# Optimization experiments

Measured on AMD Instinct MI355X. Metric: run time of the kernel, lower is better.

Reference implementation:

```python
import jax, jax.numpy as jnp
import numpy as np

B, NV, C = 4, 32768, 128
NCLS, K = 10, 500
GRID = 180  # spatial extent at feature_map_stride=8 (1440/8)
STRIDE = 8.0
PCR = np.array([-54.0, -54.0, -5.0, 54.0, 54.0, 3.0], np.float32)
VOX = np.array([0.075, 0.075, 0.2], np.float32)
LIMIT = np.array([-61.2, -61.2, -10.0, 61.2, 61.2, 10.0], np.float32)
SCORE_THRESH = 0.1
BN_EPS = 1e-5


def setup_inputs() -> dict:
    key = jax.random.key(0)
    ks = jax.random.split(key, 24)
    s = 1.0 / np.sqrt(C)
    inp = {}
    inp['feats'] = jax.random.normal(ks[0], (B * NV, C), jnp.float32)
    inp['voxel_xy'] = jax.random.randint(ks[1], (B * NV, 2), 0, GRID, dtype=jnp.int32)
    inp['W1'] = jax.random.normal(ks[2], (6, C, C), jnp.float32) * s
    inp['b1'] = jax.random.normal(ks[3], (6, C), jnp.float32) * 0.01
    inp['bn_gamma'] = 1.0 + 0.1 * jax.random.normal(ks[4], (6, C), jnp.float32)
    inp['bn_beta'] = 0.1 * jax.random.normal(ks[5], (6, C), jnp.float32)
    inp['bn_mean'] = 0.1 * jax.random.normal(ks[6], (6, C), jnp.float32)
    inp['bn_var'] = 0.5 + jax.random.uniform(ks[7], (6, C), jnp.float32)
    outs = [('hm', NCLS), ('center', 2), ('center_z', 1), ('dim', 3), ('rot', 2), ('vel', 2)]
    for i, (name, oc) in enumerate(outs):
        sc = 0.05 if name == 'dim' else s  # keep dim.exp() in a sane range
        inp['W2_' + name] = jax.random.normal(ks[8 + 2 * i], (C, oc), jnp.float32) * sc
        inp['b2_' + name] = jax.random.normal(ks[9 + 2 * i], (oc,), jnp.float32) * 0.01
    inp['batch_size'] = B
    return inp


def _forward(feats, voxel_xy, W1, b1, bn_gamma, bn_beta, bn_mean, bn_var,
             W2_hm, b2_hm, W2_center, b2_center, W2_center_z, b2_center_z,
             W2_dim, b2_dim, W2_rot, b2_rot, W2_vel, b2_vel, batch_size):
    Bs = batch_size
    N = feats.shape[0]
    Nv = N // Bs
    # --- separate heads: SubMConv2d(k=1)==per-voxel linear; BN in eval mode ---
    h = jnp.einsum('nc,bcd->bnd', feats, W1) + b1[:, None, :]            # [6,N,C]
    inv = bn_gamma / jnp.sqrt(bn_var + BN_EPS)
    h = jax.nn.relu((h - bn_mean[:, None, :]) * inv[:, None, :] + bn_beta[:, None, :])
    hm = jax.nn.sigmoid(h[0] @ W2_hm + b2_hm)                            # [N,NCLS]
    center = h[1] @ W2_center + b2_center                                # [N,2]
    center_z = h[2] @ W2_center_z + b2_center_z                          # [N,1]
    dim = jnp.exp(h[3] @ W2_dim + b2_dim)                                # [N,3]
    rot = h[4] @ W2_rot + b2_rot                                         # [N,2] (cos,sin)
    vel = h[5] @ W2_vel + b2_vel                                         # [N,2]
    # --- CenterNet-style decode (nuscenes _topk_1d): per-class topk then global topk ---
    hm_b = hm.reshape(Bs, Nv, NCLS)
    sc_c, idx_c = jax.lax.top_k(jnp.transpose(hm_b, (0, 2, 1)), K)       # [B,NCLS,K]
    topk_score, topk_ind = jax.lax.top_k(sc_c.reshape(Bs, NCLS * K), K)  # [B,K]
    class_ids = topk_ind // K                                            # [B,K]
    vox_ind = jnp.take_along_axis(idx_c.reshape(Bs, NCLS * K), topk_ind, axis=1)  # [B,K] in [0,Nv)

    def gather(x):  # x: [N,d] -> [B,K,d]
        return jnp.take_along_axis(x.reshape(Bs, Nv, -1), vox_ind[:, :, None], axis=1)

    ctr = gather(center)
    cz = gather(center_z)
    dm = gather(dim)
    rt = gather(rot)
    vl = gather(vel)
    xy = gather(voxel_xy.astype(jnp.float32))
    angle = jnp.arctan2(rt[..., 1:2], rt[..., 0:1])
    xs = (xy[..., 0:1] + ctr[..., 0:1]) * STRIDE * VOX[0] + PCR[0]
    ys = (xy[..., 1:2] + ctr[..., 1:2]) * STRIDE * VOX[1] + PCR[1]
    boxes = jnp.concatenate([xs, ys, cz, dm, angle, vl], axis=-1)        # [B,K,9]
    lim = jnp.asarray(LIMIT)
    mask = (jnp.all(boxes[..., :3] >= lim[:3], axis=-1)
            & jnp.all(boxes[..., :3] <= lim[3:], axis=-1)
            & (topk_score > SCORE_THRESH))                               # [B,K]
    boxes_scores = jnp.concatenate([boxes, topk_score[..., None]], -1) * mask[..., None].astype(boxes.dtype)
    labels = jnp.where(mask, class_ids + 1, 0)                           # class_id_mapping identity, +1
    voxel_ids = vox_ind + (jnp.arange(Bs, dtype=vox_ind.dtype) * Nv)[:, None]  # global add_features ids
    return boxes_scores, labels, voxel_ids, mask


def reference(feats, voxel_xy, W1, b1, bn_gamma, bn_beta, bn_mean, bn_var,
              W2_hm, b2_hm, W2_center, b2_center, W2_center_z, b2_center_z,
              W2_dim, b2_dim, W2_rot, b2_rot, W2_vel, b2_vel, batch_size):
    return _forward(feats, voxel_xy, W1, b1, bn_gamma, bn_beta, bn_mean, bn_var,
                    W2_hm, b2_hm, W2_center, b2_center, W2_center_z, b2_center_z,
                    W2_dim, b2_dim, W2_rot, b2_rot, W2_vel, b2_vel, batch_size)
```

## Files before the change

kernel.cpp:

```cpp
#include <hip/hip_runtime.h>
#include <math.h>

#define NV 32768
#define CD 128
#define NCLS 10
#define KSEL 500
#define BNEPS 1e-5f
#define NK (NCLS * NV)
#define H20CUT 0x3E000
#define H20BINS 6144
#define CANDCAP 2048
#define NCHUNK 64
#define CHUNKV (NK / NCHUNK)
#define CHUNK4 (CHUNKV / 4)

__global__ __launch_bounds__(256, 3) void stageA_kernel(
    const float* __restrict__ feats,
    const float* __restrict__ W1,
    const float* __restrict__ b1,
    const float* __restrict__ bng,
    const float* __restrict__ bnb,
    const float* __restrict__ bnm,
    const float* __restrict__ bnv,
    const float* __restrict__ W2hm,
    const float* __restrict__ b2hm,
    unsigned int* __restrict__ scoreb,
    unsigned int* __restrict__ zbase,
    int zwords)
{
    __shared__ __align__(16) float smem[64 * 129];
    __shared__ float w2s[CD * NCLS];
    __shared__ float b2s[NCLS];
    float4* const fsmv = (float4*)smem;

    const int tid = threadIdx.x;
    const int gbase = blockIdx.x * 64;

    if (blockIdx.x == 0) {
        for (int i = tid; i < zwords; i += 256) zbase[i] = 0u;
    }

    for (int i = tid; i < CD * NCLS; i += 256) w2s[i] = W2hm[i];
    if (tid < NCLS) b2s[tid] = b2hm[tid];

    for (int t = tid; t < 64 * 32; t += 256) {
        const int r = t >> 5;
        const int g = t & 31;
        const float4 v = *(const float4*)(feats + (((size_t)(gbase + r)) << 7) + (g << 2));
        fsmv[r * 32 + (g ^ (r & 31))] = v;
    }
    __syncthreads();

    const int c0 = (tid & 15) << 3;
    const int r0 = (tid >> 4) << 2;
    const float* const Wc0 = W1 + c0;

    float acc[4][8];
    #pragma unroll
    for (int i = 0; i < 4; ++i)
        #pragma unroll
        for (int j = 0; j < 8; ++j) acc[i][j] = 0.f;

    float4 frA[4], frB[4], wA[8], wB[8];

    #pragma unroll
    for (int i = 0; i < 4; ++i) {
        const int row = r0 + i;
        frA[i] = fsmv[row * 32 + (0 ^ (row & 31))];
    }
    #pragma unroll
    for (int kk = 0; kk < 4; ++kk) {
        wA[2 * kk]     = *(const float4*)(Wc0 + (kk << 7));
        wA[2 * kk + 1] = *(const float4*)(Wc0 + (kk << 7) + 4);
    }

#define SA_PREFETCH(FR, WW, KC)                                           \
    {                                                                     \
        const int kc_ = (KC);                                             \
        _Pragma("unroll")                                                 \
        for (int i = 0; i < 4; ++i) {                                     \
            const int row = r0 + i;                                       \
            FR[i] = fsmv[row * 32 + (kc_ ^ (row & 31))];                  \
        }                                                                 \
        const int kb_ = kc_ << 2;                                         \
        _Pragma("unroll")                                                 \
        for (int kk = 0; kk < 4; ++kk) {                                  \
            WW[2 * kk]     = *(const float4*)(Wc0 + ((kb_ + kk) << 7));   \
            WW[2 * kk + 1] = *(const float4*)(Wc0 + ((kb_ + kk) << 7) + 4); \
        }                                                                 \
    }

#define SA_COMPUTE(FR, WW)                                                \
    {                                                                     \
        const float* frp = (const float*)FR;                              \
        const float* wp  = (const float*)WW;                              \
        _Pragma("unroll")                                                 \
        for (int kk = 0; kk < 4; ++kk)                                    \
            _Pragma("unroll")                                             \
            for (int ri = 0; ri < 4; ++ri) {                              \
                const float f = frp[ri * 4 + kk];                         \
                _Pragma("unroll")                                         \
                for (int ci = 0; ci < 8; ++ci)                            \
                    acc[ri][ci] = fmaf(f, wp[kk * 8 + ci], acc[ri][ci]);  \
            }                                                             \
    }

    for (int kc = 0; kc < 32; kc += 2) {
        SA_PREFETCH(frB, wB, kc + 1)
        SA_COMPUTE(frA, wA)
        SA_PREFETCH(frA, wA, (kc + 2) & 31)
        SA_COMPUTE(frB, wB)
    }
#undef SA_PREFETCH
#undef SA_COMPUTE

    __syncthreads();

    #pragma unroll
    for (int ci = 0; ci < 8; ++ci) {
        const int c = c0 + ci;
        const float inv = bng[c] / sqrtf(bnv[c] + BNEPS);
        const float mu = bnm[c];
        const float be = bnb[c];
        const float bb = b1[c];
        #pragma unroll
        for (int ri = 0; ri < 4; ++ri) {
            const float h = (acc[ri][ci] + bb - mu) * inv + be;
            acc[ri][ci] = fmaxf(h, 0.f);
        }
    }
    #pragma unroll
    for (int ri = 0; ri < 4; ++ri)
        #pragma unroll
        for (int ci = 0; ci < 8; ++ci)
            smem[(r0 + ri) * 129 + c0 + ci] = acc[ri][ci];
    __syncthreads();

    const int r = tid & 63;
    const int ogrp = tid >> 6;
    float lg[3] = {0.f, 0.f, 0.f};
    for (int c = 0; c < 128; ++c) {
        const float a = smem[r * 129 + c];
        #pragma unroll
        for (int i = 0; i < 3; ++i) {
            const int o = ogrp + 4 * i;
            if (o < NCLS) lg[i] = fmaf(a, w2s[c * NCLS + o], lg[i]);
        }
    }
    const int n = gbase + r;
    const int b = n >> 15;
    const int v = n & (NV - 1);
    unsigned int* sb = scoreb + (size_t)b * NK;
    #pragma unroll
    for (int i = 0; i < 3; ++i) {
        const int o = ogrp + 4 * i;
        if (o < NCLS) {
            const float x = lg[i] + b2s[o];
            const float s = 1.f / (1.f + expf(-x));
            sb[o * NV + v] = __float_as_uint(s);
        }
    }
}

__global__ __launch_bounds__(256) void stageB1_kernel(
    const unsigned int* __restrict__ scoreb,
    unsigned int* __restrict__ hist20)
{
    __shared__ unsigned int lh[H20BINS];
    const int tid = threadIdx.x;
    const int b = blockIdx.y;
    const uint4* sb4 = (const uint4*)(scoreb + (size_t)b * NK) + (size_t)blockIdx.x * CHUNK4;

    for (int i = tid; i < H20BINS; i += 256) lh[i] = 0u;
    __syncthreads();

    #pragma unroll
    for (int q = 0; q < 5; ++q) {
        const uint4 v = sb4[q * 256 + tid];
        const unsigned int sv[4] = {v.x, v.y, v.z, v.w};
        #pragma unroll
        for (int k = 0; k < 4; ++k) {
            const int rel = (int)(sv[k] >> 12) - H20CUT;
            if (rel >= 0) atomicAdd(&lh[rel], 1u);
        }
    }
    __syncthreads();

    unsigned int* gh = hist20 + (size_t)b * H20BINS;
    for (int i = tid; i < H20BINS; i += 256) {
        const unsigned int v = lh[i];
        if (v) atomicAdd(&gh[i], v);
    }
}

__global__ __launch_bounds__(256) void stageB2_kernel(
    const unsigned int* __restrict__ scoreb,
    const unsigned int* __restrict__ hist20,
    unsigned int* __restrict__ cnt,
    unsigned long long* __restrict__ cand)
{
    __shared__ unsigned int hh[H20BINS];
    __shared__ unsigned int part[256];
    __shared__ unsigned int sT;
    const int tid = threadIdx.x;
    const int b = blockIdx.y;

    const unsigned int* gh = hist20 + (size_t)b * H20BINS;
    for (int i = tid; i < H20BINS; i += 256) hh[i] = gh[i];
    __syncthreads();

    unsigned int Ls = 0;
    #pragma unroll
    for (int i = 0; i < 24; ++i) Ls += hh[tid * 24 + i];
    part[tid] = Ls;
    __syncthreads();

    for (int off = 1; off < 256; off <<= 1) {
        const unsigned int add = (tid + off < 256) ? part[tid + off] : 0u;
        __syncthreads();
        part[tid] += add;
        __syncthreads();
    }
    const unsigned int incl = part[tid];
    const unsigned int above_seg = incl - Ls;

    if (above_seg < KSEL && incl >= KSEL) {
        int above = (int)above_seg;
        int tbin = tid * 24;
        for (int i = 23; i >= 0; --i) {
            const int c = (int)hh[tid * 24 + i];
            if (above + c >= KSEL) { tbin = tid * 24 + i; break; }
            above += c;
        }
        sT = ((unsigned int)(tbin + H20CUT)) << 12;
    }
    if (tid == 0 && incl < KSEL) sT = ((unsigned int)H20CUT) << 12;
    __syncthreads();
    const unsigned int T = sT;

    const uint4* sb4 = (const uint4*)(scoreb + (size_t)b * NK) + (size_t)blockIdx.x * CHUNK4;
    #pragma unroll
    for (int q = 0; q < 5; ++q) {
        const int vi = q * 256 + tid;
        const uint4 v = sb4[vi];
        const unsigned int sv[4] = {v.x, v.y, v.z, v.w};
        const unsigned int i0 = (unsigned int)((blockIdx.x * CHUNK4 + vi) * 4);
        #pragma unroll
        for (int k = 0; k < 4; ++k) {
            if (sv[k] >= T) {
                const unsigned int p = atomicAdd(&cnt[b], 1u);
                if (p < CANDCAP)
                    cand[(size_t)b * CANDCAP + p] =
                        ((unsigned long long)sv[k] << 32) |
                        (unsigned long long)(0xFFFFFFFFu - (i0 + k));
            }
        }
    }
}

__global__ __launch_bounds__(1024) void stageB3_kernel(
    const unsigned long long* __restrict__ cand,
    const unsigned int* __restrict__ cnt,
    float* __restrict__ sel_score,
    int* __restrict__ sel_cls,
    int* __restrict__ sel_vox)
{
    __shared__ unsigned long long kbuf[CANDCAP];
    const int b = blockIdx.x;
    const int tid = threadIdx.x;
    const int n = min((int)cnt[b], CANDCAP);
    int m = 512;
    while (m < n) m <<= 1;
    for (int i = tid; i < m; i += 1024)
        kbuf[i] = (i < n) ? cand[(size_t)b * CANDCAP + i] : 0ull;
    __syncthreads();
    for (int size = 2; size <= m; size <<= 1) {
        for (int stride = size >> 1; stride > 0; stride >>= 1) {
            for (int j = tid; j < m; j += 1024) {
                const int p = j ^ stride;
                if (p > j) {
                    const unsigned long long x = kbuf[j];
                    const unsigned long long y = kbuf[p];
                    const bool descRegion = ((j & size) == 0);
                    if ((x < y) == descRegion) { kbuf[j] = y; kbuf[p] = x; }
                }
            }
            __syncthreads();
        }
    }
    if (tid < KSEL) {
        const unsigned long long kk = kbuf[tid];
        const unsigned int s32 = (unsigned int)(kk >> 32);
        const unsigned int fl = 0xFFFFFFFFu - (unsigned int)(kk & 0xFFFFFFFFull);
        const int idx = b * KSEL + tid;
        sel_score[idx] = __uint_as_float(s32);
        sel_cls[idx] = (int)(fl >> 15);
        sel_vox[idx] = (int)(fl & (NV - 1));
    }
}

__global__ __launch_bounds__(640) void stageCD_kernel(
    const float* __restrict__ feats,
    const int* __restrict__ voxel_xy,
    const float* __restrict__ sel_score,
    const int* __restrict__ sel_cls,
    const int* __restrict__ sel_vox,
    const float* __restrict__ W1,
    const float* __restrict__ b1,
    const float* __restrict__ bng,
    const float* __restrict__ bnb,
    const float* __restrict__ bnm,
    const float* __restrict__ bnv,
    const float* __restrict__ W2c, const float* __restrict__ b2c,
    const float* __restrict__ W2z, const float* __restrict__ b2z,
    const float* __restrict__ W2d, const float* __restrict__ b2d,
    const float* __restrict__ W2r, const float* __restrict__ b2r,
    const float* __restrict__ W2v, const float* __restrict__ b2v,
    float* __restrict__ out,
    int total)
{
    __shared__ float fs[4][128];
    __shared__ float as_[5][4][128];
    __shared__ float dec_s[4][10];
    __shared__ int vsel[4];
    const int tid = threadIdx.x;
    const int s0 = blockIdx.x * 4;

    if (tid < 4) {
        const int s = s0 + tid;
        vsel[tid] = (s / KSEL) * NV + sel_vox[s];
    }
    __syncthreads();
    if (tid < 512) {
        const int j = tid >> 7;
        const int c = tid & 127;
        fs[j][c] = feats[((size_t)vsel[j] << 7) + c];
    }
    __syncthreads();

    {
        const int h = tid / 128;
        const int c = tid & 127;
        const int head = h + 1;
        float acc[4] = {0.f, 0.f, 0.f, 0.f};
        const float* Wh = W1 + head * (CD * CD) + c;
        for (int k = 0; k < 128; ++k) {
            const float w = Wh[k << 7];
            #pragma unroll
            for (int j = 0; j < 4; ++j)
                acc[j] = fmaf(fs[j][k], w, acc[j]);
        }
        const int hc = head * CD + c;
        const float inv = bng[hc] / sqrtf(bnv[hc] + BNEPS);
        const float mu = bnm[hc], be = bnb[hc], bb = b1[hc];
        #pragma unroll
        for (int j = 0; j < 4; ++j) {
            const float hv = (acc[j] + bb - mu) * inv + be;
            as_[h][j][c] = fmaxf(hv, 0.f);
        }
    }
    __syncthreads();

    if (tid < 40) {
        const int j = tid / 10;
        const int slot = tid % 10;
        const float* w2; const float* bb2; int hh, o, oc; bool ex = false;
        if (slot < 2)      { w2 = W2c; bb2 = b2c; hh = 0; o = slot;     oc = 2; }
        else if (slot < 3) { w2 = W2z; bb2 = b2z; hh = 1; o = 0;        oc = 1; }
        else if (slot < 6) { w2 = W2d; bb2 = b2d; hh = 2; o = slot - 3; oc = 3; ex = true; }
        else if (slot < 8) { w2 = W2r; bb2 = b2r; hh = 3; o = slot - 6; oc = 2; }
        else               { w2 = W2v; bb2 = b2v; hh = 4; o = slot - 8; oc = 2; }
        float a = 0.f;
        for (int cc = 0; cc < 128; ++cc)
            a = fmaf(as_[hh][j][cc], w2[cc * oc + o], a);
        a += bb2[o];
        if (ex) a = expf(a);
        dec_s[j][slot] = a;
    }
    __syncthreads();

    if (tid < 4) {
        const int s = s0 + tid;
        const int b = s / KSEL;
        const float score = sel_score[s];
        const int cls = sel_cls[s];
        const int v = sel_vox[s];
        const int n = b * NV + v;
        const float xi = (float)voxel_xy[2 * n];
        const float yi = (float)voxel_xy[2 * n + 1];
        const float* dd = dec_s[tid];
        const float cx = dd[0], cy = dd[1], cz = dd[2];
        const float d0 = dd[3], d1 = dd[4], d2 = dd[5];
        const float rc = dd[6], rs = dd[7], ve0 = dd[8], ve1 = dd[9];
        const float SV = 0.075f * 8.0f;
        const float xs = (xi + cx) * SV + (-54.0f);
        const float ys = (yi + cy) * SV + (-54.0f);
        const float ang = atan2f(rs, rc);
        const bool mk = (xs >= -61.2f) && (ys >= -61.2f) && (cz >= -10.0f) &&
                        (xs <= 61.2f) && (ys <= 61.2f) && (cz <= 10.0f) &&
                        (score > 0.1f);
        const float m = mk ? 1.f : 0.f;
        float* bx = out + (size_t)s * 10;
        bx[0] = xs * m; bx[1] = ys * m; bx[2] = cz * m;
        bx[3] = d0 * m; bx[4] = d1 * m; bx[5] = d2 * m;
        bx[6] = ang * m; bx[7] = ve0 * m; bx[8] = ve1 * m; bx[9] = score * m;
        out[(size_t)total * 10 + s] = mk ? (float)(cls + 1) : 0.f;
        out[(size_t)total * 11 + s] = (float)n;
        out[(size_t)total * 12 + s] = m;
    }
}

extern "C" void kernel_launch(void* const* d_in, const int* in_sizes, int n_in,
                              void* d_out, int out_size, void* d_ws, size_t ws_size,
                              hipStream_t stream) {
    const float* feats   = (const float*)d_in[0];
    const int*   voxelxy = (const int*)d_in[1];
    const float* W1   = (const float*)d_in[2];
    const float* b1   = (const float*)d_in[3];
    const float* bng  = (const float*)d_in[4];
    const float* bnb  = (const float*)d_in[5];
    const float* bnm  = (const float*)d_in[6];
    const float* bnv  = (const float*)d_in[7];
    const float* W2hm = (const float*)d_in[8];
    const float* b2hm = (const float*)d_in[9];
    const float* W2c  = (const float*)d_in[10];
    const float* b2c  = (const float*)d_in[11];
    const float* W2z  = (const float*)d_in[12];
    const float* b2z  = (const float*)d_in[13];
    const float* W2d  = (const float*)d_in[14];
    const float* b2d  = (const float*)d_in[15];
    const float* W2r  = (const float*)d_in[16];
    const float* b2r  = (const float*)d_in[17];
    const float* W2v  = (const float*)d_in[18];
    const float* b2v  = (const float*)d_in[19];

    const int B = in_sizes[0] / (NV * CD);
    const int N = B * NV;
    const int total = B * KSEL;

    char* ws = (char*)d_ws;
    unsigned int* scoreb = (unsigned int*)ws;            ws += (size_t)B * NK * 4;
    unsigned int* hist20 = (unsigned int*)ws;            ws += (size_t)B * H20BINS * 4;
    unsigned int* cnt    = (unsigned int*)ws;            ws += 8 * 4;
    unsigned long long* cand = (unsigned long long*)ws;  ws += (size_t)B * CANDCAP * 8;
    float* sel_score = (float*)ws;                       ws += (size_t)total * 4;
    int*   sel_cls   = (int*)ws;                         ws += (size_t)total * 4;
    int*   sel_vox   = (int*)ws;                         ws += (size_t)total * 4;

    const int zwords = B * H20BINS + 8;

    stageA_kernel<<<dim3(N / 64), dim3(256), 0, stream>>>(
        feats, W1, b1, bng, bnb, bnm, bnv, W2hm, b2hm, scoreb, hist20, zwords);

    stageB1_kernel<<<dim3(NCHUNK, B), dim3(256), 0, stream>>>(scoreb, hist20);
    stageB2_kernel<<<dim3(NCHUNK, B), dim3(256), 0, stream>>>(scoreb, hist20, cnt, cand);
    stageB3_kernel<<<dim3(B), dim3(1024), 0, stream>>>(
        cand, cnt, sel_score, sel_cls, sel_vox);

    stageCD_kernel<<<dim3(total / 4), dim3(640), 0, stream>>>(
        feats, voxelxy, sel_score, sel_cls, sel_vox,
        W1, b1, bng, bnb, bnm, bnv,
        W2c, b2c, W2z, b2z, W2d, b2d, W2r, b2r, W2v, b2v,
        (float*)d_out, total);
}
```

Before: 274.3 us.

## Restructure top-k threshold selection with per-block histograms and LDS-staged candidate compaction

Histogram blocks now write private partial histograms instead of global atomics, and a new single-block-per-batch kernel reduces them and computes the threshold once rather than in every chunk block. Candidate compaction stages hits in shared memory and reserves global slots with one atomic per block instead of one per hit. Chunk count is halved, so each block does more work, and stageA's occupancy hint rises while it no longer zeroes the histogram. This adds an extra kernel launch and a serial 32-partial reduction in exchange for less global atomic contention and no redundant threshold computation.

```diff
diff --git a/kernel.cpp b/kernel.cpp
--- a/kernel.cpp
+++ b/kernel.cpp
@@ -10,11 +10,12 @@
 #define H20CUT 0x3E000
 #define H20BINS 6144
 #define CANDCAP 2048
-#define NCHUNK 64
-#define CHUNKV (NK / NCHUNK)
-#define CHUNK4 (CHUNKV / 4)
-
-__global__ __launch_bounds__(256, 3) void stageA_kernel(
+#define NP 32
+#define PCHUNKV (NK / NP)
+#define PCHUNK4 (PCHUNKV / 4)
+#define LCAP 512
+
+__global__ __launch_bounds__(256, 4) void stageA_kernel(
     const float* __restrict__ feats,
     const float* __restrict__ W1,
     const float* __restrict__ b1,
@@ -24,9 +25,7 @@
     const float* __restrict__ bnv,
     const float* __restrict__ W2hm,
     const float* __restrict__ b2hm,
-    unsigned int* __restrict__ scoreb,
-    unsigned int* __restrict__ zbase,
-    int zwords)
+    unsigned int* __restrict__ scoreb)
 {
     __shared__ __align__(16) float smem[64 * 129];
     __shared__ float w2s[CD * NCLS];
@@ -35,10 +34,6 @@
 
     const int tid = threadIdx.x;
     const int gbase = blockIdx.x * 64;
-
-    if (blockIdx.x == 0) {
-        for (int i = tid; i < zwords; i += 256) zbase[i] = 0u;
-    }
 
     for (int i = tid; i < CD * NCLS; i += 256) w2s[i] = W2hm[i];
     if (tid < NCLS) b2s[tid] = b2hm[tid];
@@ -164,18 +159,18 @@
 
 __global__ __launch_bounds__(256) void stageB1_kernel(
     const unsigned int* __restrict__ scoreb,
-    unsigned int* __restrict__ hist20)
+    unsigned int* __restrict__ hist_part)
 {
     __shared__ unsigned int lh[H20BINS];
     const int tid = threadIdx.x;
     const int b = blockIdx.y;
-    const uint4* sb4 = (const uint4*)(scoreb + (size_t)b * NK) + (size_t)blockIdx.x * CHUNK4;
+    const uint4* sb4 = (const uint4*)(scoreb + (size_t)b * NK) + (size_t)blockIdx.x * PCHUNK4;
 
     for (int i = tid; i < H20BINS; i += 256) lh[i] = 0u;
     __syncthreads();
 
     #pragma unroll
-    for (int q = 0; q < 5; ++q) {
+    for (int q = 0; q < 10; ++q) {
         const uint4 v = sb4[q * 256 + tid];
         const unsigned int sv[4] = {v.x, v.y, v.z, v.w};
         #pragma unroll
@@ -186,37 +181,35 @@
     }
     __syncthreads();
 
-    unsigned int* gh = hist20 + (size_t)b * H20BINS;
-    for (int i = tid; i < H20BINS; i += 256) {
-        const unsigned int v = lh[i];
-        if (v) atomicAdd(&gh[i], v);
-    }
-}
-
-__global__ __launch_bounds__(256) void stageB2_kernel(
-    const unsigned int* __restrict__ scoreb,
-    const unsigned int* __restrict__ hist20,
-    unsigned int* __restrict__ cnt,
-    unsigned long long* __restrict__ cand)
-{
-    __shared__ unsigned int hh[H20BINS];
-    __shared__ unsigned int part[256];
+    unsigned int* gh = hist_part + ((size_t)b * NP + blockIdx.x) * H20BINS;
+    for (int i = tid; i < H20BINS; i += 256) gh[i] = lh[i];
+}
+
+__global__ __launch_bounds__(1024) void stageB2_kernel(
+    const unsigned int* __restrict__ hist_part,
+    unsigned int* __restrict__ Tbuf,
+    unsigned int* __restrict__ cnt)
+{
+    __shared__ unsigned int part[1024];
     __shared__ unsigned int sT;
-    const int tid = threadIdx.x;
-    const int b = blockIdx.y;
-
-    const unsigned int* gh = hist20 + (size_t)b * H20BINS;
-    for (int i = tid; i < H20BINS; i += 256) hh[i] = gh[i];
-    __syncthreads();
-
+    const int b = blockIdx.x;
+    const int tid = threadIdx.x;
+
+    unsigned int loc[6] = {0u, 0u, 0u, 0u, 0u, 0u};
+    const unsigned int* hp = hist_part + (size_t)b * NP * H20BINS;
+    for (int p = 0; p < NP; ++p) {
+        const unsigned int* hq = hp + (size_t)p * H20BINS + tid * 6;
+        #pragma unroll
+        for (int i = 0; i < 6; ++i) loc[i] += hq[i];
+    }
     unsigned int Ls = 0;
     #pragma unroll
-    for (int i = 0; i < 24; ++i) Ls += hh[tid * 24 + i];
+    for (int i = 0; i < 6; ++i) Ls += loc[i];
     part[tid] = Ls;
     __syncthreads();
 
-    for (int off = 1; off < 256; off <<= 1) {
-        const unsigned int add = (tid + off < 256) ? part[tid + off] : 0u;
+    for (int off = 1; off < 1024; off <<= 1) {
+        const unsigned int add = (tid + off < 1024) ? part[tid + off] : 0u;
         __syncthreads();
         part[tid] += add;
         __syncthreads();
@@ -226,39 +219,77 @@
 
     if (above_seg < KSEL && incl >= KSEL) {
         int above = (int)above_seg;
-        int tbin = tid * 24;
-        for (int i = 23; i >= 0; --i) {
-            const int c = (int)hh[tid * 24 + i];
-            if (above + c >= KSEL) { tbin = tid * 24 + i; break; }
-            above += c;
+        int tbin = -1;
+        #pragma unroll
+        for (int i = 5; i >= 0; --i) {
+            const int cbin = (int)loc[i];
+            if (tbin < 0) {
+                if (above + cbin >= KSEL) tbin = tid * 6 + i;
+                else above += cbin;
+            }
         }
         sT = ((unsigned int)(tbin + H20CUT)) << 12;
     }
-    if (tid == 0 && incl < KSEL) sT = ((unsigned int)H20CUT) << 12;
-    __syncthreads();
-    const unsigned int T = sT;
-
-    const uint4* sb4 = (const uint4*)(scoreb + (size_t)b * NK) + (size_t)blockIdx.x * CHUNK4;
-    #pragma unroll
-    for (int q = 0; q < 5; ++q) {
+    if (tid == 0 && part[0] < KSEL) sT = ((unsigned int)H20CUT) << 12;
+    __syncthreads();
+    if (tid == 0) {
+        Tbuf[b] = sT;
+        cnt[b] = 0u;
+    }
+}
+
+__global__ __launch_bounds__(256) void stageB3_kernel(
+    const unsigned int* __restrict__ scoreb,
+    const unsigned int* __restrict__ Tbuf,
+    unsigned int* __restrict__ cnt,
+    unsigned long long* __restrict__ cand)
+{
+    __shared__ unsigned long long lbuf[LCAP];
+    __shared__ unsigned int lcnt;
+    __shared__ unsigned int sbase;
+    const int tid = threadIdx.x;
+    const int b = blockIdx.y;
+    const unsigned int T = Tbuf[b];
+    const uint4* sb4 = (const uint4*)(scoreb + (size_t)b * NK) + (size_t)blockIdx.x * PCHUNK4;
+    unsigned long long* cb = cand + (size_t)b * CANDCAP;
+
+    if (tid == 0) lcnt = 0u;
+    __syncthreads();
+
+    #pragma unroll
+    for (int q = 0; q < 10; ++q) {
         const int vi = q * 256 + tid;
         const uint4 v = sb4[vi];
         const unsigned int sv[4] = {v.x, v.y, v.z, v.w};
-        const unsigned int i0 = (unsigned int)((blockIdx.x * CHUNK4 + vi) * 4);
+        const unsigned int i0 = (unsigned int)((blockIdx.x * PCHUNK4 + vi) * 4);
         #pragma unroll
         for (int k = 0; k < 4; ++k) {
             if (sv[k] >= T) {
-                const unsigned int p = atomicAdd(&cnt[b], 1u);
-                if (p < CANDCAP)
-                    cand[(size_t)b * CANDCAP + p] =
-                        ((unsigned long long)sv[k] << 32) |
-                        (unsigned long long)(0xFFFFFFFFu - (i0 + k));
+                const unsigned long long key =
+                    ((unsigned long long)sv[k] << 32) |
+                    (unsigned long long)(0xFFFFFFFFu - (i0 + k));
+                const unsigned int p = atomicAdd(&lcnt, 1u);
+                if (p < LCAP) {
+                    lbuf[p] = key;
+                } else {
+                    const unsigned int gp = atomicAdd(&cnt[b], 1u);
+                    if (gp < CANDCAP) cb[gp] = key;
+                }
             }
         }
     }
-}
-
-__global__ __launch_bounds__(1024) void stageB3_kernel(
+    __syncthreads();
+    const unsigned int nloc = min(lcnt, (unsigned int)LCAP);
+    if (tid == 0) sbase = (nloc > 0u) ? atomicAdd(&cnt[b], nloc) : 0u;
+    __syncthreads();
+    const unsigned int base = sbase;
+    for (unsigned int i = tid; i < nloc; i += 256) {
+        const unsigned int pos = base + i;
+        if (pos < CANDCAP) cb[pos] = lbuf[i];
+    }
+}
+
+__global__ __launch_bounds__(1024) void stageB4_kernel(
     const unsigned long long* __restrict__ cand,
     const unsigned int* __restrict__ cnt,
     float* __restrict__ sel_score,
@@ -439,22 +470,22 @@
     const int total = B * KSEL;
 
     char* ws = (char*)d_ws;
-    unsigned int* scoreb = (unsigned int*)ws;            ws += (size_t)B * NK * 4;
-    unsigned int* hist20 = (unsigned int*)ws;            ws += (size_t)B * H20BINS * 4;
-    unsigned int* cnt    = (unsigned int*)ws;            ws += 8 * 4;
+    unsigned int* scoreb    = (unsigned int*)ws;         ws += (size_t)B * NK * 4;
+    unsigned int* hist_part = (unsigned int*)ws;         ws += (size_t)B * NP * H20BINS * 4;
+    unsigned int* cnt       = (unsigned int*)ws;         ws += 8 * 4;
+    unsigned int* Tbuf      = (unsigned int*)ws;         ws += 8 * 4;
     unsigned long long* cand = (unsigned long long*)ws;  ws += (size_t)B * CANDCAP * 8;
     float* sel_score = (float*)ws;                       ws += (size_t)total * 4;
     int*   sel_cls   = (int*)ws;                         ws += (size_t)total * 4;
     int*   sel_vox   = (int*)ws;                         ws += (size_t)total * 4;
 
-    const int zwords = B * H20BINS + 8;
-
     stageA_kernel<<<dim3(N / 64), dim3(256), 0, stream>>>(
-        feats, W1, b1, bng, bnb, bnm, bnv, W2hm, b2hm, scoreb, hist20, zwords);
-
-    stageB1_kernel<<<dim3(NCHUNK, B), dim3(256), 0, stream>>>(scoreb, hist20);
-    stageB2_kernel<<<dim3(NCHUNK, B), dim3(256), 0, stream>>>(scoreb, hist20, cnt, cand);
-    stageB3_kernel<<<dim3(B), dim3(1024), 0, stream>>>(
+        feats, W1, b1, bng, bnb, bnm, bnv, W2hm, b2hm, scoreb);
+
+    stageB1_kernel<<<dim3(NP, B), dim3(256), 0, stream>>>(scoreb, hist_part);
+    stageB2_kernel<<<dim3(B), dim3(1024), 0, stream>>>(hist_part, Tbuf, cnt);
+    stageB3_kernel<<<dim3(NP, B), dim3(256), 0, stream>>>(scoreb, Tbuf, cnt, cand);
+    stageB4_kernel<<<dim3(B), dim3(1024), 0, stream>>>(
         cand, cnt, sel_score, sel_cls, sel_vox);
 
     stageCD_kernel<<<dim3(total / 4), dim3(640), 0, stream>>>(
```

New measurement: 274.1 us. Within noise of the previous version (-0.1%).

## Fuse histogram into stage A and merge candidate gather with last-block sort

Applied to the files above, without the earlier changes.

The score histogram is now built with global atomics directly in the stage A epilogue, which removes the separate pass that re-read all scores. The candidate-gather and bitonic-sort kernels are merged into one kernel. It collects candidates in a per-block shared buffer, and a ticket counter lets the last block per batch do the sort. Zeroing moves to a hipMemsetAsync, and stage A's occupancy hint is raised to 4 blocks per CU. The trade-offs are heavy global atomic contention on high-score histogram bins and a sort that now runs serially in a single 256-thread block.

```diff
diff --git a/kernel.cpp b/kernel.cpp
--- a/kernel.cpp
+++ b/kernel.cpp
@@ -10,11 +10,12 @@
 #define H20CUT 0x3E000
 #define H20BINS 6144
 #define CANDCAP 2048
-#define NCHUNK 64
-#define CHUNKV (NK / NCHUNK)
-#define CHUNK4 (CHUNKV / 4)
-
-__global__ __launch_bounds__(256, 3) void stageA_kernel(
+#define NP 32
+#define PCHUNKV (NK / NP)
+#define PCHUNK4 (PCHUNKV / 4)
+#define LCAP 512
+
+__global__ __launch_bounds__(256, 4) void stageA_kernel(
     const float* __restrict__ feats,
     const float* __restrict__ W1,
     const float* __restrict__ b1,
@@ -25,8 +26,7 @@
     const float* __restrict__ W2hm,
     const float* __restrict__ b2hm,
     unsigned int* __restrict__ scoreb,
-    unsigned int* __restrict__ zbase,
-    int zwords)
+    unsigned int* __restrict__ hist20)
 {
     __shared__ __align__(16) float smem[64 * 129];
     __shared__ float w2s[CD * NCLS];
@@ -35,10 +35,6 @@
 
     const int tid = threadIdx.x;
     const int gbase = blockIdx.x * 64;
-
-    if (blockIdx.x == 0) {
-        for (int i = tid; i < zwords; i += 256) zbase[i] = 0u;
-    }
 
     for (int i = tid; i < CD * NCLS; i += 256) w2s[i] = W2hm[i];
     if (tid < NCLS) b2s[tid] = b2hm[tid];
@@ -151,70 +147,52 @@
     const int b = n >> 15;
     const int v = n & (NV - 1);
     unsigned int* sb = scoreb + (size_t)b * NK;
+    unsigned int* hb = hist20 + (size_t)b * H20BINS;
     #pragma unroll
     for (int i = 0; i < 3; ++i) {
         const int o = ogrp + 4 * i;
         if (o < NCLS) {
             const float x = lg[i] + b2s[o];
             const float s = 1.f / (1.f + expf(-x));
-            sb[o * NV + v] = __float_as_uint(s);
+            const unsigned int bits = __float_as_uint(s);
+            sb[o * NV + v] = bits;
+            const int rel = (int)(bits >> 12) - H20CUT;
+            if (rel >= 0) atomicAdd(&hb[rel], 1u);
         }
     }
 }
 
-__global__ __launch_bounds__(256) void stageB1_kernel(
-    const unsigned int* __restrict__ scoreb,
-    unsigned int* __restrict__ hist20)
-{
-    __shared__ unsigned int lh[H20BINS];
-    const int tid = threadIdx.x;
-    const int b = blockIdx.y;
-    const uint4* sb4 = (const uint4*)(scoreb + (size_t)b * NK) + (size_t)blockIdx.x * CHUNK4;
-
-    for (int i = tid; i < H20BINS; i += 256) lh[i] = 0u;
-    __syncthreads();
-
-    #pragma unroll
-    for (int q = 0; q < 5; ++q) {
-        const uint4 v = sb4[q * 256 + tid];
-        const unsigned int sv[4] = {v.x, v.y, v.z, v.w};
-        #pragma unroll
-        for (int k = 0; k < 4; ++k) {
-            const int rel = (int)(sv[k] >> 12) - H20CUT;
-            if (rel >= 0) atomicAdd(&lh[rel], 1u);
-        }
-    }
-    __syncthreads();
-
-    unsigned int* gh = hist20 + (size_t)b * H20BINS;
-    for (int i = tid; i < H20BINS; i += 256) {
-        const unsigned int v = lh[i];
-        if (v) atomicAdd(&gh[i], v);
-    }
-}
-
-__global__ __launch_bounds__(256) void stageB2_kernel(
+__global__ __launch_bounds__(256) void stageBF_kernel(
     const unsigned int* __restrict__ scoreb,
     const unsigned int* __restrict__ hist20,
     unsigned int* __restrict__ cnt,
-    unsigned long long* __restrict__ cand)
+    unsigned int* __restrict__ ticket,
+    unsigned long long* __restrict__ cand,
+    float* __restrict__ sel_score,
+    int* __restrict__ sel_cls,
+    int* __restrict__ sel_vox)
 {
-    __shared__ unsigned int hh[H20BINS];
+    __shared__ union {
+        unsigned int lh[H20BINS];
+        unsigned long long kbuf[CANDCAP];
+    } u;
+    __shared__ unsigned long long lbuf[LCAP];
     __shared__ unsigned int part[256];
-    __shared__ unsigned int sT;
+    __shared__ unsigned int sT, lcnt, sbase, slast;
+
     const int tid = threadIdx.x;
     const int b = blockIdx.y;
 
     const unsigned int* gh = hist20 + (size_t)b * H20BINS;
-    for (int i = tid; i < H20BINS; i += 256) hh[i] = gh[i];
+    for (int i = tid; i < H20BINS; i += 256) u.lh[i] = gh[i];
+    if (tid == 0) lcnt = 0u;
     __syncthreads();
 
     unsigned int Ls = 0;
     #pragma unroll
-    for (int i = 0; i < 24; ++i) Ls += hh[tid * 24 + i];
+    for (int i = 0; i < 24; ++i) Ls += u.lh[tid * 24 + i];
     part[tid] = Ls;
     __syncthreads();
-
     for (int off = 1; off < 256; off <<= 1) {
         const unsigned int add = (tid + off < 256) ? part[tid + off] : 0u;
         __syncthreads();
@@ -223,76 +201,86 @@
     }
     const unsigned int incl = part[tid];
     const unsigned int above_seg = incl - Ls;
-
     if (above_seg < KSEL && incl >= KSEL) {
         int above = (int)above_seg;
         int tbin = tid * 24;
         for (int i = 23; i >= 0; --i) {
-            const int c = (int)hh[tid * 24 + i];
+            const int c = (int)u.lh[tid * 24 + i];
             if (above + c >= KSEL) { tbin = tid * 24 + i; break; }
             above += c;
         }
         sT = ((unsigned int)(tbin + H20CUT)) << 12;
     }
-    if (tid == 0 && incl < KSEL) sT = ((unsigned int)H20CUT) << 12;
+    if (tid == 0 && part[0] < KSEL) sT = ((unsigned int)H20CUT) << 12;
     __syncthreads();
     const unsigned int T = sT;
 
-    const uint4* sb4 = (const uint4*)(scoreb + (size_t)b * NK) + (size_t)blockIdx.x * CHUNK4;
-    #pragma unroll
-    for (int q = 0; q < 5; ++q) {
+    const uint4* sb4 = (const uint4*)(scoreb + (size_t)b * NK) + (size_t)blockIdx.x * PCHUNK4;
+    unsigned long long* cb = cand + (size_t)b * CANDCAP;
+    #pragma unroll
+    for (int q = 0; q < 10; ++q) {
         const int vi = q * 256 + tid;
         const uint4 v = sb4[vi];
         const unsigned int sv[4] = {v.x, v.y, v.z, v.w};
-        const unsigned int i0 = (unsigned int)((blockIdx.x * CHUNK4 + vi) * 4);
+        const unsigned int i0 = (unsigned int)((blockIdx.x * PCHUNK4 + vi) * 4);
         #pragma unroll
         for (int k = 0; k < 4; ++k) {
             if (sv[k] >= T) {
-                const unsigned int p = atomicAdd(&cnt[b], 1u);
-                if (p < CANDCAP)
-                    cand[(size_t)b * CANDCAP + p] =
-                        ((unsigned long long)sv[k] << 32) |
-                        (unsigned long long)(0xFFFFFFFFu - (i0 + k));
+                const unsigned long long key =
+                    ((unsigned long long)sv[k] << 32) |
+                    (unsigned long long)(0xFFFFFFFFu - (i0 + k));
+                const unsigned int p = atomicAdd(&lcnt, 1u);
+                if (p < LCAP) {
+                    lbuf[p] = key;
+                } else {
+                    const unsigned int gp = atomicAdd(&cnt[b], 1u);
+                    if (gp < CANDCAP) cb[gp] = key;
+                }
             }
         }
     }
-}
-
-__global__ __launch_bounds__(1024) void stageB3_kernel(
-    const unsigned long long* __restrict__ cand,
-    const unsigned int* __restrict__ cnt,
-    float* __restrict__ sel_score,
-    int* __restrict__ sel_cls,
-    int* __restrict__ sel_vox)
-{
-    __shared__ unsigned long long kbuf[CANDCAP];
-    const int b = blockIdx.x;
-    const int tid = threadIdx.x;
-    const int n = min((int)cnt[b], CANDCAP);
+    __syncthreads();
+    const unsigned int nloc = min(lcnt, (unsigned int)LCAP);
+    if (tid == 0) sbase = (nloc > 0u) ? atomicAdd(&cnt[b], nloc) : 0u;
+    __syncthreads();
+    const unsigned int base = sbase;
+    for (unsigned int i = tid; i < nloc; i += 256) {
+        const unsigned int pos = base + i;
+        if (pos < CANDCAP) cb[pos] = lbuf[i];
+    }
+    __syncthreads();
+
+    __threadfence();
+    if (tid == 0) slast = atomicAdd(&ticket[b], 1u);
+    __syncthreads();
+    if (slast != (unsigned int)(NP - 1)) return;
+
+    __threadfence();
+    const int n = min((int)atomicAdd(&cnt[b], 0u), CANDCAP);
     int m = 512;
     while (m < n) m <<= 1;
-    for (int i = tid; i < m; i += 1024)
-        kbuf[i] = (i < n) ? cand[(size_t)b * CANDCAP + i] : 0ull;
+    for (int i = tid; i < m; i += 256)
+        u.kbuf[i] = (i < n) ? cb[i] : 0ull;
     __syncthreads();
     for (int size = 2; size <= m; size <<= 1) {
         for (int stride = size >> 1; stride > 0; stride >>= 1) {
-            for (int j = tid; j < m; j += 1024) {
+            for (int j = tid; j < m; j += 256) {
                 const int p = j ^ stride;
                 if (p > j) {
-                    const unsigned long long x = kbuf[j];
-                    const unsigned long long y = kbuf[p];
+                    const unsigned long long x = u.kbuf[j];
+                    const unsigned long long y = u.kbuf[p];
                     const bool descRegion = ((j & size) == 0);
-                    if ((x < y) == descRegion) { kbuf[j] = y; kbuf[p] = x; }
+                    if ((x < y) == descRegion) { u.kbuf[j] = y; u.kbuf[p] = x; }
                 }
             }
             __syncthreads();
         }
     }
-    if (tid < KSEL) {
-        const unsigned long long kk = kbuf[tid];
+    for (int i = tid; i < KSEL; i += 256) {
+        const unsigned long long kk = u.kbuf[i];
         const unsigned int s32 = (unsigned int)(kk >> 32);
         const unsigned int fl = 0xFFFFFFFFu - (unsigned int)(kk & 0xFFFFFFFFull);
-        const int idx = b * KSEL + tid;
+        const int idx = b * KSEL + i;
         sel_score[idx] = __uint_as_float(s32);
         sel_cls[idx] = (int)(fl >> 15);
         sel_vox[idx] = (int)(fl & (NV - 1));
@@ -442,20 +430,19 @@
     unsigned int* scoreb = (unsigned int*)ws;            ws += (size_t)B * NK * 4;
     unsigned int* hist20 = (unsigned int*)ws;            ws += (size_t)B * H20BINS * 4;
     unsigned int* cnt    = (unsigned int*)ws;            ws += 8 * 4;
+    unsigned int* ticket = (unsigned int*)ws;            ws += 8 * 4;
     unsigned long long* cand = (unsigned long long*)ws;  ws += (size_t)B * CANDCAP * 8;
     float* sel_score = (float*)ws;                       ws += (size_t)total * 4;
     int*   sel_cls   = (int*)ws;                         ws += (size_t)total * 4;
     int*   sel_vox   = (int*)ws;                         ws += (size_t)total * 4;
 
-    const int zwords = B * H20BINS + 8;
+    hipMemsetAsync(hist20, 0, ((size_t)B * H20BINS + 16) * 4, stream);
 
     stageA_kernel<<<dim3(N / 64), dim3(256), 0, stream>>>(
-        feats, W1, b1, bng, bnb, bnm, bnv, W2hm, b2hm, scoreb, hist20, zwords);
-
-    stageB1_kernel<<<dim3(NCHUNK, B), dim3(256), 0, stream>>>(scoreb, hist20);
-    stageB2_kernel<<<dim3(NCHUNK, B), dim3(256), 0, stream>>>(scoreb, hist20, cnt, cand);
-    stageB3_kernel<<<dim3(B), dim3(1024), 0, stream>>>(
-        cand, cnt, sel_score, sel_cls, sel_vox);
+        feats, W1, b1, bng, bnb, bnm, bnv, W2hm, b2hm, scoreb, hist20);
+
+    stageBF_kernel<<<dim3(NP, B), dim3(256), 0, stream>>>(
+        scoreb, hist20, cnt, ticket, cand, sel_score, sel_cls, sel_vox);
 
     stageCD_kernel<<<dim3(total / 4), dim3(640), 0, stream>>>(
         feats, voxelxy, sel_score, sel_cls, sel_vox,
```

New measurement: 345.8 us. 26.1% more time.
